# Kernel tuning notes

Measured on AMD Instinct MI355X. Metric: run time of the kernel, lower is better.

The kernel has to match this reference:

```python
import jax, jax.numpy as jnp
import numpy as np

N_EMBD = 1024
HEAD_SIZE = 64

def setup_inputs() -> dict:
    key = jax.random.key(0)
    kx, kk, kq, kv = jax.random.split(key, 4)
    x = jax.random.normal(kx, (8, 2048, N_EMBD), dtype=jnp.float32)
    # torch nn.Linear(n_embd, head_size, bias=False): y = x @ W.T, W:[head_size,n_embd].
    # We store the transposed form [n_embd, head_size] directly.
    s = 1.0 / np.sqrt(N_EMBD)
    Wk = jax.random.uniform(kk, (N_EMBD, HEAD_SIZE), jnp.float32, -s, s)
    Wq = jax.random.uniform(kq, (N_EMBD, HEAD_SIZE), jnp.float32, -s, s)
    Wv = jax.random.uniform(kv, (N_EMBD, HEAD_SIZE), jnp.float32, -s, s)
    return {"x": x, "Wk": Wk, "Wq": Wq, "Wv": Wv}

def reference(x, Wk, Wq, Wv):
    B, T, C = x.shape
    k = jnp.einsum('btc,cd->btd', x, Wk)  # [B,T,d]
    q = jnp.einsum('btc,cd->btd', x, Wq)
    v = jnp.einsum('btc,cd->btd', x, Wv)
    d = k.shape[-1]
    wei = jnp.einsum('btd,bsd->bts', q, k) * (d ** -0.5)  # [B,T,T]
    causal = jnp.tril(jnp.ones((T, T), dtype=bool))
    wei = jnp.where(causal, wei, -jnp.inf)
    wei = jax.nn.softmax(wei, axis=-1)
    # dropout p=0.0 -> identity (eval-mode equivalent)
    out = jnp.einsum('bts,bsd->btd', wei, v)  # [B,T,d]
    return out
```

## Files before the change

kernel.cpp:

```cpp
#include <hip/hip_runtime.h>
#include <hip/hip_bf16.h>

#define TB 8
#define TT 2048
#define TC 1024
#define TD 64
#define PSP 72

typedef __attribute__((ext_vector_type(8))) short bf16x8;
typedef __attribute__((ext_vector_type(4))) float f32x4;

__device__ __forceinline__ short f2bf(float f) {
    union { float f; unsigned u; } v; v.f = f;
    unsigned r = v.u + 0x7fffu + ((v.u >> 16) & 1u);
    return (short)(r >> 16);
}

__device__ __forceinline__ unsigned pk2(float a, float b) {
    __hip_bfloat162 h = __float22bfloat162_rn(make_float2(a, b));
    union { __hip_bfloat162 h2; unsigned u; } c; c.h2 = h;
    return c.u;
}

__device__ __forceinline__ void gl_lds16(const void* g, void* l) {
    __builtin_amdgcn_global_load_lds(
        (const __attribute__((address_space(1))) unsigned*)g,
        (__attribute__((address_space(3))) unsigned*)l, 16, 0, 0);
}

__global__ __launch_bounds__(256) void convert_w(const float* __restrict__ Wk,
                                                 const float* __restrict__ Wq,
                                                 const float* __restrict__ Wv,
                                                 short* __restrict__ Wt) {
    __shared__ short Tl[64 * PSP];
    const int tid = threadIdx.x;
    const int kc  = blockIdx.x;
    const int oid = blockIdx.y;
    const float* src = (oid == 0) ? Wk : (oid == 1) ? Wq : Wv;
    const float scale = (oid == 1) ? 0.125f : 1.0f;
    const int row = tid >> 2;
    const int c0  = (tid & 3) << 4;

    const float* sp = src + (size_t)(kc * 64 + row) * TD + c0;
    float4 a = ((const float4*)sp)[0], b = ((const float4*)sp)[1];
    float4 c = ((const float4*)sp)[2], d = ((const float4*)sp)[3];
    float vals[16] = {a.x,a.y,a.z,a.w, b.x,b.y,b.z,b.w,
                      c.x,c.y,c.z,c.w, d.x,d.y,d.z,d.w};
#pragma unroll
    for (int j = 0; j < 16; ++j)
        Tl[(c0 + j) * PSP + row] = f2bf(vals[j] * scale);
    __syncthreads();

    const int n  = tid >> 2;
    const int k0 = (tid & 3) << 4;
    uint4 u0 = *(uint4*)&Tl[n * PSP + k0];
    uint4 u1 = *(uint4*)&Tl[n * PSP + k0 + 8];
    uint4* dst = (uint4*)(Wt + (size_t)(oid * 64 + n) * TC + kc * 64 + k0);
    dst[0] = u0; dst[1] = u1;
}

__global__ __launch_bounds__(256, 3) void qkv_proj(const float* __restrict__ x,
                                                   const short* __restrict__ Wt,
                                                   short* __restrict__ qb,
                                                   short* __restrict__ kb,
                                                   short* __restrict__ vt) {
    __shared__ __align__(16) float xs[64 * 64];
    const int tid = threadIdx.x;
    const int bid = blockIdx.x;
    const int oid = (bid >> 3) % 3;
    const int mg  = (bid / 24) * 8 + (bid & 7);
    const int wv  = tid >> 6, lane = tid & 63;
    const int wu  = __builtin_amdgcn_readfirstlane(wv);
    const int l15 = lane & 15, quad = lane >> 4;

    f32x4 acc[4];
#pragma unroll
    for (int i = 0; i < 4; ++i) acc[i] = (f32x4){0.f, 0.f, 0.f, 0.f};

    const float* xtile = x + (size_t)mg * 64 * TC;
    const short* wbase = Wt + (size_t)(oid * 64 + l15) * TC + quad * 8;

    for (int k0 = 0; k0 < TC; k0 += 64) {
        __syncthreads();
#pragma unroll
        for (int j = 0; j < 4; ++j) {
            int sbase = (j * 4 + wu) * 64;
            int sl = sbase + lane;
            int row = sl >> 4, g = sl & 15;
            int gg = g ^ (row & 15);
            gl_lds16(xtile + (size_t)row * TC + k0 + gg * 4, xs + sbase * 4);
        }
        __syncthreads();

        const int xrow = (wv * 16 + l15) * 16;
        bf16x8 A[2];
#pragma unroll
        for (int k32 = 0; k32 < 2; ++k32) {
            int G = k32 * 8 + quad * 2;
            float4 f0 = *(const float4*)(xs + (xrow + (G ^ l15)) * 4);
            float4 f1 = *(const float4*)(xs + (xrow + ((G + 1) ^ l15)) * 4);
            union { bf16x8 v; unsigned u[4]; } pk;
            pk.u[0] = pk2(f0.x, f0.y); pk.u[1] = pk2(f0.z, f0.w);
            pk.u[2] = pk2(f1.x, f1.y); pk.u[3] = pk2(f1.z, f1.w);
            A[k32] = pk.v;
        }
#pragma unroll
        for (int nt = 0; nt < 4; ++nt) {
            bf16x8 b0 = *(const bf16x8*)(wbase + (size_t)nt * 16 * TC + k0);
            bf16x8 b1 = *(const bf16x8*)(wbase + (size_t)nt * 16 * TC + k0 + 32);
            acc[nt] = __builtin_amdgcn_mfma_f32_16x16x32_bf16(A[0], b0, acc[nt], 0, 0, 0);
            acc[nt] = __builtin_amdgcn_mfma_f32_16x16x32_bf16(A[1], b1, acc[nt], 0, 0, 0);
        }
    }

    const int row0 = mg * 64 + wv * 16;
    if (oid == 2) {
        const int bb = row0 >> 11;
        const int t0 = (row0 & 2047) + quad * 4;
#pragma unroll
        for (int nt = 0; nt < 4; ++nt) {
            int d = nt * 16 + l15;
            alignas(8) short t4[4];
#pragma unroll
            for (int r = 0; r < 4; ++r) t4[r] = f2bf(acc[nt][r]);
            *(uint2*)(vt + (size_t)(bb * TD + d) * TT + t0) = *(uint2*)t4;
        }
    } else {
        short* dst = (oid == 0) ? kb : qb;
#pragma unroll
        for (int nt = 0; nt < 4; ++nt)
#pragma unroll
            for (int r = 0; r < 4; ++r)
                dst[(size_t)(row0 + quad * 4 + r) * TD + nt * 16 + l15] = f2bf(acc[nt][r]);
    }
}

__global__ __launch_bounds__(256, 3) void attn(const short* __restrict__ qb,
                                               const short* __restrict__ kb,
                                               const short* __restrict__ vt,
                                               float* __restrict__ out) {
    __shared__ __align__(16) char smem[41984];
    short* Ksb = (short*)smem;
    short* Vsb = (short*)(smem + 16384);
    short* Ps  = (short*)(smem + 32768);
    float* Os  = (float*)smem;
    float* ls  = (float*)(smem + 16384);

    const int tid = threadIdx.x;
    const int it  = (int)gridDim.x - 1 - (int)blockIdx.x;
    const int b   = blockIdx.y;
    const int wv  = tid >> 6, lane = tid & 63;
    const int wu  = __builtin_amdgcn_readfirstlane(wv);
    const int l15 = lane & 15, quad = lane >> 4;
    const int qh  = wv >> 1;
    const int ks  = wv & 1;
    const int q0  = it * 32;
    const int KT  = (it >> 1) + 1;
    const float L2E = 1.4426950408889634f;

    const size_t qoff = (size_t)(b * TT + q0 + qh * 16 + l15) * TD + quad * 8;
    bf16x8 aq0 = *(const bf16x8*)(qb + qoff);
    bf16x8 aq1 = *(const bf16x8*)(qb + qoff + 32);

    f32x4 O[4];
#pragma unroll
    for (int i = 0; i < 4; ++i) O[i] = (f32x4){0.f, 0.f, 0.f, 0.f};
    float lsum[4] = {0.f, 0.f, 0.f, 0.f};

    const short* kbb = kb + (size_t)b * TT * TD;
    const short* vbb = vt + (size_t)b * TD * TT;
    short* myPs = Ps + wu * (16 * PSP);

    for (int kt0 = 0; kt0 < KT; kt0 += 2) {
        __syncthreads();
#pragma unroll
        for (int h = 0; h < 2; ++h) {
            int kt = kt0 + h;
            if (kt >= KT) break;
#pragma unroll
            for (int j = 0; j < 2; ++j) {
                int sbase = (j * 4 + wu) * 64;
                int sl = sbase + lane;
                int row = sl >> 3, g = sl & 7;
                int gg = g ^ (row & 7);
                gl_lds16(kbb + (size_t)(kt * 64 + row) * TD + gg * 8,
                         Ksb + h * 4096 + sbase * 8);
                gl_lds16(vbb + (size_t)row * TT + kt * 64 + gg * 8,
                         Vsb + h * 4096 + sbase * 8);
            }
        }
        __syncthreads();

        const int mykt = kt0 + ks;
        if (mykt < KT) {
            const short* Kt = Ksb + ks * 4096;
            const short* Vt = Vsb + ks * 4096;
            f32x4 S[4];
#pragma unroll
            for (int nt = 0; nt < 4; ++nt) {
                int row = nt * 16 + l15, r7 = l15 & 7;
                bf16x8 b0 = *(const bf16x8*)(Kt + row * 64 + (quad ^ r7) * 8);
                bf16x8 b1 = *(const bf16x8*)(Kt + row * 64 + ((4 + quad) ^ r7) * 8);
                S[nt] = (f32x4){0.f, 0.f, 0.f, 0.f};
                S[nt] = __builtin_amdgcn_mfma_f32_16x16x32_bf16(aq0, b0, S[nt], 0, 0, 0);
                S[nt] = __builtin_amdgcn_mfma_f32_16x16x32_bf16(aq1, b1, S[nt], 0, 0, 0);
            }
            const bool diag = (mykt == KT - 1);
            const int qrow = q0 + qh * 16 + quad * 4;
#pragma unroll
            for (int nt = 0; nt < 4; ++nt) {
                int scol = mykt * 64 + nt * 16 + l15;
#pragma unroll
                for (int r = 0; r < 4; ++r) {
                    float p = exp2f(S[nt][r] * L2E);
                    if (diag && (scol > qrow + r)) p = 0.f;
                    lsum[r] += p;
                    myPs[(quad * 4 + r) * PSP + nt * 16 + l15] = f2bf(p);
                }
            }
            bf16x8 p0 = *(const bf16x8*)(myPs + l15 * PSP + quad * 8);
            bf16x8 p1 = *(const bf16x8*)(myPs + l15 * PSP + quad * 8 + 32);
#pragma unroll
            for (int dt = 0; dt < 4; ++dt) {
                int row = dt * 16 + l15, r7 = l15 & 7;
                bf16x8 b0 = *(const bf16x8*)(Vt + row * 64 + (quad ^ r7) * 8);
                bf16x8 b1 = *(const bf16x8*)(Vt + row * 64 + ((4 + quad) ^ r7) * 8);
                O[dt] = __builtin_amdgcn_mfma_f32_16x16x32_bf16(p0, b0, O[dt], 0, 0, 0);
                O[dt] = __builtin_amdgcn_mfma_f32_16x16x32_bf16(p1, b1, O[dt], 0, 0, 0);
            }
        }
    }
    __syncthreads();

#pragma unroll
    for (int r = 0; r < 4; ++r) {
        float v = lsum[r];
        v += __shfl_xor(v, 1); v += __shfl_xor(v, 2);
        v += __shfl_xor(v, 4); v += __shfl_xor(v, 8);
        lsum[r] = v;
    }
#pragma unroll
    for (int dt = 0; dt < 4; ++dt)
#pragma unroll
        for (int r = 0; r < 4; ++r)
            Os[(wv * 16 + quad * 4 + r) * 64 + dt * 16 + l15] = O[dt][r];
    if (l15 == 0)
#pragma unroll
        for (int r = 0; r < 4; ++r) ls[wv * 16 + quad * 4 + r] = lsum[r];
    __syncthreads();

    const int col = tid & 63;
    for (int rr = tid >> 6; rr < 32; rr += 4) {
        int h = rr >> 4, r16 = rr & 15;
        float o = Os[((2 * h)     * 16 + r16) * 64 + col]
                + Os[((2 * h + 1) * 16 + r16) * 64 + col];
        float L = ls[(2 * h) * 16 + r16] + ls[(2 * h + 1) * 16 + r16];
        out[(size_t)(b * TT + q0 + rr) * TD + col] = o / L;
    }
}

extern "C" void kernel_launch(void* const* d_in, const int* in_sizes, int n_in,
                              void* d_out, int out_size, void* d_ws, size_t ws_size,
                              hipStream_t stream) {
    const float* x  = (const float*)d_in[0];
    const float* Wk = (const float*)d_in[1];
    const float* Wq = (const float*)d_in[2];
    const float* Wv = (const float*)d_in[3];
    float* out = (float*)d_out;

    char* ws = (char*)d_ws;
    short* Wt = (short*)(ws);
    short* qb = (short*)(ws + 524288);
    short* kb = (short*)(ws + 2621440);
    short* vt = (short*)(ws + 4718592);

    convert_w<<<dim3(16, 3), dim3(256), 0, stream>>>(Wk, Wq, Wv, Wt);
    qkv_proj<<<dim3(768), dim3(256), 0, stream>>>(x, Wt, qb, kb, vt);
    attn<<<dim3(64, 8), dim3(256), 0, stream>>>(qb, kb, vt, out);
}
```

Measured before the change: 170.9 us.

## Double-buffer global-to-LDS loads in projection and attention, keep weights in registers

Both kernels now prefetch the next K-chunk (projection) or next pair of KV tiles (attention) into a second LDS buffer while computing on the current one. Raw barriers and explicit vmcnt waits replace __syncthreads. The projection also preloads each wave's full weight slice into 32 registers and remaps waves to output columns. Attention moves to a 1D grid that interleaves batches so the heaviest query tiles launch first. LDS use doubles and the occupancy hint drops from 3 to 2 blocks, trading occupancy for overlap. The hand-written vmcnt(8) waits rely on exact in-flight load counts: attention issues 8 loads per wave per stage, but projection issues 8 per thread per stage plus a separate 32-load weight preload, which raises correctness risk.

```diff
diff --git a/kernel.cpp b/kernel.cpp
--- a/kernel.cpp
+++ b/kernel.cpp
@@ -27,6 +27,10 @@
         (const __attribute__((address_space(1))) unsigned*)g,
         (__attribute__((address_space(3))) unsigned*)l, 16, 0, 0);
 }
+
+__device__ __forceinline__ void bar_raw()  { asm volatile("s_barrier" ::: "memory"); }
+__device__ __forceinline__ void wait_vm8() { asm volatile("s_waitcnt vmcnt(8)" ::: "memory"); }
+__device__ __forceinline__ void wait_vm0() { asm volatile("s_waitcnt vmcnt(0)" ::: "memory"); }
 
 __global__ __launch_bounds__(256) void convert_w(const float* __restrict__ Wk,
                                                  const float* __restrict__ Wq,
@@ -59,12 +63,12 @@
     dst[0] = u0; dst[1] = u1;
 }
 
-__global__ __launch_bounds__(256, 3) void qkv_proj(const float* __restrict__ x,
+__global__ __launch_bounds__(256, 2) void qkv_proj(const float* __restrict__ x,
                                                    const short* __restrict__ Wt,
                                                    short* __restrict__ qb,
                                                    short* __restrict__ kb,
                                                    short* __restrict__ vt) {
-    __shared__ __align__(16) float xs[64 * 64];
+    __shared__ __align__(16) float xs[2][64 * 128];
     const int tid = threadIdx.x;
     const int bid = blockIdx.x;
     const int oid = (bid >> 3) % 3;
@@ -73,82 +77,96 @@
     const int wu  = __builtin_amdgcn_readfirstlane(wv);
     const int l15 = lane & 15, quad = lane >> 4;
 
+    bf16x8 Bf[32];
+    const short* wrow = Wt + (size_t)(oid * 64 + wv * 16 + l15) * TC + quad * 8;
+#pragma unroll
+    for (int s = 0; s < 32; ++s)
+        Bf[s] = *(const bf16x8*)(wrow + s * 32);
+    wait_vm0();
+
     f32x4 acc[4];
 #pragma unroll
     for (int i = 0; i < 4; ++i) acc[i] = (f32x4){0.f, 0.f, 0.f, 0.f};
 
     const float* xtile = x + (size_t)mg * 64 * TC;
-    const short* wbase = Wt + (size_t)(oid * 64 + l15) * TC + quad * 8;
-
-    for (int k0 = 0; k0 < TC; k0 += 64) {
-        __syncthreads();
-#pragma unroll
-        for (int j = 0; j < 4; ++j) {
-            int sbase = (j * 4 + wu) * 64;
-            int sl = sbase + lane;
-            int row = sl >> 4, g = sl & 15;
-            int gg = g ^ (row & 15);
-            gl_lds16(xtile + (size_t)row * TC + k0 + gg * 4, xs + sbase * 4);
+
+#define STAGE_X(r)                                                          \
+    {                                                                       \
+        float* dstb = &xs[(r) & 1][0];                                      \
+        _Pragma("unroll")                                                   \
+        for (int j = 0; j < 8; ++j) {                                       \
+            int sbase = (j * 4 + wu) * 64;                                  \
+            int sl = sbase + lane;                                          \
+            int rw = sl >> 5, g = sl & 31;                                  \
+            int gg = g ^ (rw & 15);                                         \
+            gl_lds16(xtile + (size_t)rw * TC + (r) * 128 + gg * 4,          \
+                     dstb + (size_t)sbase * 4);                             \
+        }                                                                   \
+    }
+
+    STAGE_X(0);
+    for (int r = 0; r < 8; ++r) {
+        if (r < 7) { STAGE_X(r + 1); wait_vm8(); }
+        else       { wait_vm0(); }
+        bar_raw();
+        const float* xb = &xs[r & 1][0];
+#pragma unroll
+        for (int sl = 0; sl < 4; ++sl) {
+#pragma unroll
+            for (int mt = 0; mt < 4; ++mt) {
+                int rw = mt * 16 + l15;
+                int gg = sl * 8 + quad * 2;
+                float4 f0 = *(const float4*)(xb + (rw * 32 + (gg ^ l15)) * 4);
+                float4 f1 = *(const float4*)(xb + (rw * 32 + ((gg + 1) ^ l15)) * 4);
+                union { bf16x8 v; unsigned u[4]; } pk;
+                pk.u[0] = pk2(f0.x, f0.y); pk.u[1] = pk2(f0.z, f0.w);
+                pk.u[2] = pk2(f1.x, f1.y); pk.u[3] = pk2(f1.z, f1.w);
+                acc[mt] = __builtin_amdgcn_mfma_f32_16x16x32_bf16(
+                              pk.v, Bf[r * 4 + sl], acc[mt], 0, 0, 0);
+            }
         }
-        __syncthreads();
-
-        const int xrow = (wv * 16 + l15) * 16;
-        bf16x8 A[2];
-#pragma unroll
-        for (int k32 = 0; k32 < 2; ++k32) {
-            int G = k32 * 8 + quad * 2;
-            float4 f0 = *(const float4*)(xs + (xrow + (G ^ l15)) * 4);
-            float4 f1 = *(const float4*)(xs + (xrow + ((G + 1) ^ l15)) * 4);
-            union { bf16x8 v; unsigned u[4]; } pk;
-            pk.u[0] = pk2(f0.x, f0.y); pk.u[1] = pk2(f0.z, f0.w);
-            pk.u[2] = pk2(f1.x, f1.y); pk.u[3] = pk2(f1.z, f1.w);
-            A[k32] = pk.v;
-        }
-#pragma unroll
-        for (int nt = 0; nt < 4; ++nt) {
-            bf16x8 b0 = *(const bf16x8*)(wbase + (size_t)nt * 16 * TC + k0);
-            bf16x8 b1 = *(const bf16x8*)(wbase + (size_t)nt * 16 * TC + k0 + 32);
-            acc[nt] = __builtin_amdgcn_mfma_f32_16x16x32_bf16(A[0], b0, acc[nt], 0, 0, 0);
-            acc[nt] = __builtin_amdgcn_mfma_f32_16x16x32_bf16(A[1], b1, acc[nt], 0, 0, 0);
-        }
-    }
-
-    const int row0 = mg * 64 + wv * 16;
+        bar_raw();
+    }
+#undef STAGE_X
+
+    const int row0 = mg * 64;
     if (oid == 2) {
         const int bb = row0 >> 11;
-        const int t0 = (row0 & 2047) + quad * 4;
-#pragma unroll
-        for (int nt = 0; nt < 4; ++nt) {
-            int d = nt * 16 + l15;
+        const int d  = wv * 16 + l15;
+#pragma unroll
+        for (int mt = 0; mt < 4; ++mt) {
+            int t0 = (row0 & 2047) + mt * 16 + quad * 4;
             alignas(8) short t4[4];
 #pragma unroll
-            for (int r = 0; r < 4; ++r) t4[r] = f2bf(acc[nt][r]);
+            for (int r = 0; r < 4; ++r) t4[r] = f2bf(acc[mt][r]);
             *(uint2*)(vt + (size_t)(bb * TD + d) * TT + t0) = *(uint2*)t4;
         }
     } else {
         short* dst = (oid == 0) ? kb : qb;
 #pragma unroll
-        for (int nt = 0; nt < 4; ++nt)
+        for (int mt = 0; mt < 4; ++mt)
 #pragma unroll
             for (int r = 0; r < 4; ++r)
-                dst[(size_t)(row0 + quad * 4 + r) * TD + nt * 16 + l15] = f2bf(acc[nt][r]);
-    }
-}
-
-__global__ __launch_bounds__(256, 3) void attn(const short* __restrict__ qb,
+                dst[(size_t)(row0 + mt * 16 + quad * 4 + r) * TD + wv * 16 + l15]
+                    = f2bf(acc[mt][r]);
+    }
+}
+
+__global__ __launch_bounds__(256, 2) void attn(const short* __restrict__ qb,
                                                const short* __restrict__ kb,
                                                const short* __restrict__ vt,
                                                float* __restrict__ out) {
-    __shared__ __align__(16) char smem[41984];
-    short* Ksb = (short*)smem;
-    short* Vsb = (short*)(smem + 16384);
-    short* Ps  = (short*)(smem + 32768);
-    float* Os  = (float*)smem;
-    float* ls  = (float*)(smem + 16384);
+    __shared__ __align__(16) char smem[74752];
+    short* Ks = (short*)smem;
+    short* Vs = (short*)(smem + 32768);
+    short* Ps = (short*)(smem + 65536);
+    float* Os = (float*)smem;
+    float* ls = (float*)(smem + 16384);
 
     const int tid = threadIdx.x;
-    const int it  = (int)gridDim.x - 1 - (int)blockIdx.x;
-    const int b   = blockIdx.y;
+    const int pm  = blockIdx.x;
+    const int b   = pm & 7;
+    const int it  = 63 - (pm >> 3);
     const int wv  = tid >> 6, lane = tid & 63;
     const int wu  = __builtin_amdgcn_readfirstlane(wv);
     const int l15 = lane & 15, quad = lane >> 4;
@@ -156,11 +174,13 @@
     const int ks  = wv & 1;
     const int q0  = it * 32;
     const int KT  = (it >> 1) + 1;
+    const int R   = (KT + 1) >> 1;
     const float L2E = 1.4426950408889634f;
 
     const size_t qoff = (size_t)(b * TT + q0 + qh * 16 + l15) * TD + quad * 8;
     bf16x8 aq0 = *(const bf16x8*)(qb + qoff);
     bf16x8 aq1 = *(const bf16x8*)(qb + qoff + 32);
+    wait_vm0();
 
     f32x4 O[4];
 #pragma unroll
@@ -171,36 +191,43 @@
     const short* vbb = vt + (size_t)b * TD * TT;
     short* myPs = Ps + wu * (16 * PSP);
 
-    for (int kt0 = 0; kt0 < KT; kt0 += 2) {
-        __syncthreads();
-#pragma unroll
-        for (int h = 0; h < 2; ++h) {
-            int kt = kt0 + h;
-            if (kt >= KT) break;
-#pragma unroll
-            for (int j = 0; j < 2; ++j) {
-                int sbase = (j * 4 + wu) * 64;
-                int sl = sbase + lane;
-                int row = sl >> 3, g = sl & 7;
-                int gg = g ^ (row & 7);
-                gl_lds16(kbb + (size_t)(kt * 64 + row) * TD + gg * 8,
-                         Ksb + h * 4096 + sbase * 8);
-                gl_lds16(vbb + (size_t)row * TT + kt * 64 + gg * 8,
-                         Vsb + h * 4096 + sbase * 8);
-            }
-        }
-        __syncthreads();
-
-        const int mykt = kt0 + ks;
+#define STAGE_KV(r)                                                         \
+    {                                                                       \
+        short* kdst = Ks + ((r) & 1) * 8192;                                \
+        short* vdst = Vs + ((r) & 1) * 8192;                                \
+        _Pragma("unroll")                                                   \
+        for (int h = 0; h < 2; ++h) {                                       \
+            int kt = 2 * (r) + h; if (kt > KT - 1) kt = KT - 1;             \
+            _Pragma("unroll")                                               \
+            for (int j = 0; j < 2; ++j) {                                   \
+                int sbase = (j * 4 + wu) * 64;                              \
+                int sl = sbase + lane;                                      \
+                int rw = sl >> 3, g = sl & 7;                               \
+                int gg = g ^ (rw & 7);                                      \
+                gl_lds16(kbb + (size_t)(kt * 64 + rw) * TD + gg * 8,        \
+                         kdst + h * 4096 + sbase * 8);                      \
+                gl_lds16(vbb + (size_t)rw * TT + kt * 64 + gg * 8,          \
+                         vdst + h * 4096 + sbase * 8);                      \
+            }                                                               \
+        }                                                                   \
+    }
+
+    STAGE_KV(0);
+    for (int r = 0; r < R; ++r) {
+        if (r + 1 < R) { STAGE_KV(r + 1); wait_vm8(); }
+        else           { wait_vm0(); }
+        bar_raw();
+
+        const int mykt = 2 * r + ks;
         if (mykt < KT) {
-            const short* Kt = Ksb + ks * 4096;
-            const short* Vt = Vsb + ks * 4096;
+            const short* Kt = Ks + (r & 1) * 8192 + ks * 4096;
+            const short* Vt = Vs + (r & 1) * 8192 + ks * 4096;
             f32x4 S[4];
 #pragma unroll
             for (int nt = 0; nt < 4; ++nt) {
-                int row = nt * 16 + l15, r7 = l15 & 7;
-                bf16x8 b0 = *(const bf16x8*)(Kt + row * 64 + (quad ^ r7) * 8);
-                bf16x8 b1 = *(const bf16x8*)(Kt + row * 64 + ((4 + quad) ^ r7) * 8);
+                int rw = nt * 16 + l15, r7 = l15 & 7;
+                bf16x8 b0 = *(const bf16x8*)(Kt + rw * 64 + (quad ^ r7) * 8);
+                bf16x8 b1 = *(const bf16x8*)(Kt + rw * 64 + ((4 + quad) ^ r7) * 8);
                 S[nt] = (f32x4){0.f, 0.f, 0.f, 0.f};
                 S[nt] = __builtin_amdgcn_mfma_f32_16x16x32_bf16(aq0, b0, S[nt], 0, 0, 0);
                 S[nt] = __builtin_amdgcn_mfma_f32_16x16x32_bf16(aq1, b1, S[nt], 0, 0, 0);
@@ -211,25 +238,27 @@
             for (int nt = 0; nt < 4; ++nt) {
                 int scol = mykt * 64 + nt * 16 + l15;
 #pragma unroll
-                for (int r = 0; r < 4; ++r) {
-                    float p = exp2f(S[nt][r] * L2E);
-                    if (diag && (scol > qrow + r)) p = 0.f;
-                    lsum[r] += p;
-                    myPs[(quad * 4 + r) * PSP + nt * 16 + l15] = f2bf(p);
+                for (int r4 = 0; r4 < 4; ++r4) {
+                    float p = exp2f(S[nt][r4] * L2E);
+                    if (diag && (scol > qrow + r4)) p = 0.f;
+                    lsum[r4] += p;
+                    myPs[(quad * 4 + r4) * PSP + nt * 16 + l15] = f2bf(p);
                 }
             }
             bf16x8 p0 = *(const bf16x8*)(myPs + l15 * PSP + quad * 8);
             bf16x8 p1 = *(const bf16x8*)(myPs + l15 * PSP + quad * 8 + 32);
 #pragma unroll
             for (int dt = 0; dt < 4; ++dt) {
-                int row = dt * 16 + l15, r7 = l15 & 7;
-                bf16x8 b0 = *(const bf16x8*)(Vt + row * 64 + (quad ^ r7) * 8);
-                bf16x8 b1 = *(const bf16x8*)(Vt + row * 64 + ((4 + quad) ^ r7) * 8);
+                int rw = dt * 16 + l15, r7 = l15 & 7;
+                bf16x8 b0 = *(const bf16x8*)(Vt + rw * 64 + (quad ^ r7) * 8);
+                bf16x8 b1 = *(const bf16x8*)(Vt + rw * 64 + ((4 + quad) ^ r7) * 8);
                 O[dt] = __builtin_amdgcn_mfma_f32_16x16x32_bf16(p0, b0, O[dt], 0, 0, 0);
                 O[dt] = __builtin_amdgcn_mfma_f32_16x16x32_bf16(p1, b1, O[dt], 0, 0, 0);
             }
         }
-    }
+        bar_raw();
+    }
+#undef STAGE_KV
     __syncthreads();
 
 #pragma unroll
@@ -276,5 +305,5 @@
 
     convert_w<<<dim3(16, 3), dim3(256), 0, stream>>>(Wk, Wq, Wv, Wt);
     qkv_proj<<<dim3(768), dim3(256), 0, stream>>>(x, Wt, qb, kb, vt);
-    attn<<<dim3(64, 8), dim3(256), 0, stream>>>(qb, kb, vt, out);
-}
+    attn<<<dim3(512), dim3(256), 0, stream>>>(qb, kb, vt, out);
+}
```

Result: slower. 179.3 us (+4.9%).
